# Performance work log

Measured on AMD Instinct MI355X. Metric: run time of the kernel, lower is better.

Reference implementation:

```python
import jax, jax.numpy as jnp
import numpy as np

# ---- SLAYER neuron / simulation params (network.yaml equivalents) ----
THETA = 10.0       # spiking threshold
TAU_SR = 10.0      # synaptic (PSP) alpha-kernel time constant
TAU_REF = 1.0      # refractory alpha-kernel time constant
SCALE_REF = 2.0
TS = 1.0           # simulation step
T_SAMPLE = 350     # number of timesteps

B, NIN, NHID, NOUT = 32, 2312, 512, 10


def _alpha_kernel(tau, mult=1.0, eps=0.01):
    # mirrors slayer._calculateAlphaKernel truncation rule
    ks = []
    for t in np.arange(0.0, T_SAMPLE, TS):
        v = mult * t / tau * np.exp(1.0 - t / tau)
        if abs(v) < eps and t > tau:
            break
        ks.append(v)
    return jnp.asarray(np.asarray(ks, dtype=np.float32))

SRM_KERNEL = _alpha_kernel(TAU_SR)                        # truncated PSP kernel
D_REF = float(np.exp(-TS / TAU_REF))                      # geometric decay of refractory alpha kernel
C_REF = float(-SCALE_REF * THETA * np.e * TS / TAU_REF)   # refKernel[j] = C_REF * j * D_REF**j


def psp(x):
    # causal temporal conv with the SRM alpha kernel, scaled by Ts. x: (B, C, T)
    b, c, t = x.shape
    k = SRM_KERNEL.shape[0]
    out = jax.lax.conv_general_dilated(
        x.reshape(b * c, 1, t), SRM_KERNEL[::-1].reshape(1, 1, k),
        window_strides=(1,), padding=[(k - 1, 0)])
    return (out * TS).reshape(b, c, t)


def spike(u_psp):
    # Sequential thresholding with FULL refractory recurrence: a spike at time s
    # adds refKernel[n-s] = C_REF*(n-s)*D_REF**(n-s) to all future potentials.
    # The alpha kernel is realized EXACTLY by a 2-state linear recurrence (x, y):
    #   x[n] = sum_s spk[s] * d^(n-s),  y[n] = sum_s spk[s] * (n-s) * d^(n-s)
    def step(carry, p_t):
        x, y = carry
        y = D_REF * (y + x)
        u = p_t + C_REF * y           # membrane potential after refractory response
        spk = (u >= THETA).astype(p_t.dtype)
        x = D_REF * x + spk
        return (x, y), spk / TS       # SLAYER emits spikes of magnitude 1/Ts
    b, c, _ = u_psp.shape
    init = (jnp.zeros((b, c), u_psp.dtype), jnp.zeros((b, c), u_psp.dtype))
    _, s = jax.lax.scan(step, init, jnp.moveaxis(u_psp, -1, 0))
    return jnp.moveaxis(s, 0, -1)


def setup_inputs() -> dict:
    key = jax.random.key(0)
    k1, k2, k3 = jax.random.split(key, 3)
    spikeInput = (jax.random.uniform(k1, (B, NIN, T_SAMPLE)) < 0.03).astype(jnp.float32) / TS
    W1 = jax.random.normal(k2, (NHID, NIN), jnp.float32) * 0.05
    W2 = jax.random.normal(k3, (NOUT, NHID), jnp.float32) * 0.5
    return {"spikeInput": spikeInput, "W1": W1, "W2": W2}


def reference(spikeInput, W1, W2):
    # fc (1x1x1 conv == per-timestep matmul) -> psp -> spike, twice
    s1 = spike(psp(jnp.einsum('oi,bit->bot', W1, spikeInput)))
    s2 = spike(psp(jnp.einsum('oi,bit->bot', W2, s1)))
    return s2
```

## Files before the change

kernel.cpp:

```cpp
#include <hip/hip_runtime.h>
#include <hip/hip_bf16.h>
#include <math.h>

#define B_    32
#define NIN_  2312
#define NHID_ 512
#define NOUT_ 10
#define T_    350
#define KLEN  77
#define MW    40
#define NIB   37
#define NTB   6
#define MAXA2 320

__global__ __launch_bounds__(256) void w1t_k(const float* __restrict__ W,
                                             float* __restrict__ WT) {
  __shared__ float tile[32][33];
  int i0 = blockIdx.x * 32, o0 = blockIdx.y * 32;
  int tx = threadIdx.x, tyb = threadIdx.y;
#pragma unroll
  for (int s = 0; s < 4; ++s) {
    int ty = tyb + s * 8;
    int o = o0 + ty, i = i0 + tx;
    if (i < NIN_) tile[ty][tx] = W[(size_t)o * NIN_ + i];
  }
  __syncthreads();
#pragma unroll
  for (int s = 0; s < 4; ++s) {
    int ty = tyb + s * 8;
    int i = i0 + ty, o = o0 + tx;
    if (i < NIN_) WT[(size_t)i * NHID_ + o] = tile[tx][ty];
  }
}

__global__ __launch_bounds__(256) void inmask_k(const float* __restrict__ X,
                                                unsigned long long* __restrict__ msk) {
  __shared__ unsigned evens[64], odds[64];
  int blk = blockIdx.x;
  int iblk = blk % NIB;
  int b = blk / NIB;
  int tid = threadIdx.x;
  int w = tid >> 6, lane = tid & 63;
  int rhalf = lane >> 5;
  int c2 = lane & 31;
  const float* base = X + ((size_t)b * NIN_ + (size_t)iblk * 64) * T_;
  for (int tb = 0; tb < NTB; ++tb) {
    int tbase = tb * 64;
#define PH1_(Q)                                                                \
  {                                                                            \
    int row = 16 * w + 2 * (Q) + rhalf;                                        \
    bool ok = (iblk * 64 + row) < NIN_ && (tbase + 2 * c2) < T_;               \
    const float* rp = base + (size_t)row * T_ + tbase + 2 * c2;                \
    float2 v = ok ? *(const float2*)rp : make_float2(0.f, 0.f);                \
    unsigned long long be = __ballot(v.x != 0.f);                              \
    unsigned long long bo = __ballot(v.y != 0.f);                              \
    if (lane == 0) {                                                           \
      evens[16 * w + 2 * (Q)] = (unsigned)be;                                  \
      odds[16 * w + 2 * (Q)] = (unsigned)bo;                                   \
    }                                                                          \
    if (lane == 1) {                                                           \
      evens[16 * w + 2 * (Q) + 1] = (unsigned)(be >> 32);                      \
      odds[16 * w + 2 * (Q) + 1] = (unsigned)(bo >> 32);                       \
    }                                                                          \
  }
    PH1_(0) PH1_(1) PH1_(2) PH1_(3) PH1_(4) PH1_(5) PH1_(6) PH1_(7)
#undef PH1_
    __syncthreads();
    unsigned ev = evens[lane], od = odds[lane];
    unsigned long long* mrow =
        msk + ((size_t)b * T_ + tbase + w * 16) * MW + iblk;
#define BAL_(P)                                                                \
  {                                                                            \
    unsigned sel = ((P) & 1) ? od : ev;                                        \
    unsigned long long bw_ =                                                   \
        __ballot(((sel >> (w * 8 + ((P) >> 1))) & 1u) != 0u);                  \
    if (lane == (P) && (tbase + w * 16 + (P)) < T_)                            \
      mrow[(size_t)(P) * MW] = bw_;                                            \
  }
    BAL_(0)  BAL_(1)  BAL_(2)  BAL_(3)  BAL_(4)  BAL_(5)  BAL_(6)  BAL_(7)
    BAL_(8)  BAL_(9)  BAL_(10) BAL_(11) BAL_(12) BAL_(13) BAL_(14) BAL_(15)
#undef BAL_
    __syncthreads();
  }
}

__global__ __launch_bounds__(64) void accum1_k(const unsigned long long* __restrict__ msk,
                                               const float* __restrict__ WT,
                                               float* __restrict__ Z1) {
  __shared__ unsigned short list[MAXA2];
  int id = blockIdx.x;
  int bt = id >> 1, oc = id & 1;
  int lane = threadIdx.x;
  unsigned long long wm = (lane < NIB) ? msk[(size_t)bt * MW + lane] : 0ull;
  int pc = __popcll(wm);
  int pre = pc;
#pragma unroll
  for (int d = 1; d < 64; d <<= 1) {
    int o = __shfl_up(pre, d);
    if (lane >= d) pre += o;
  }
  int base = pre - pc;
  int n = __shfl(pre, 63);
  while (wm) {
    int j = __builtin_ctzll(wm);
    if (base < MAXA2) list[base] = (unsigned short)(lane * 64 + j);
    ++base;
    wm &= wm - 1;
  }
  __syncthreads();
  if (n > MAXA2) n = MAXA2;
  const float4* wbase = (const float4*)WT + (size_t)oc * 64 + lane;
  float4 acc = make_float4(0.f, 0.f, 0.f, 0.f);
#pragma unroll 16
  for (int j = 0; j < n; ++j) {
    float4 v = wbase[(size_t)list[j] * (NHID_ / 4)];
    acc.x += v.x;
    acc.y += v.y;
    acc.z += v.z;
    acc.w += v.w;
  }
  ((float4*)(Z1 + (size_t)bt * NHID_))[(size_t)oc * 64 + lane] = acc;
}

__global__ __launch_bounds__(64) void scan1_k(const float* __restrict__ Z1,
                                              unsigned long long* __restrict__ mask) {
  int lane = threadIdx.x;
  int b = blockIdx.x >> 3, g = blockIdx.x & 7;
  int h = g * 64 + lane;
  const double dp   = exp(-0.1);
  const double Ap   = exp(1.0) / 10.0;
  const double D77  = exp(-7.7);
  const float  Dref = (float)exp(-1.0);
  const float  Cref = (float)(-20.0 * exp(1.0));
  double Xc = 0.0, Yc = 0.0, Xd = 0.0, Yd = 0.0;
  float xr = 0.f, yr = 0.f;
  const float* zb = Z1 + (size_t)b * T_ * NHID_ + h;
  unsigned long long* mb = mask + (size_t)b * T_ * 8 + g;
  for (int t0 = 0; t0 < T_; t0 += 16) {
    float z[16], zd[16];
#pragma unroll
    for (int k = 0; k < 16; ++k) {
      int t = t0 + k;
      z[k]  = (t < T_) ? zb[(size_t)t * NHID_] : 0.f;
      zd[k] = (t >= KLEN && t < T_) ? zb[(size_t)(t - KLEN) * NHID_] : 0.f;
    }
#pragma unroll
    for (int k = 0; k < 16; ++k) {
      int t = t0 + k;
      if (t >= T_) break;
      Yc = dp * (Yc + Xc); Xc = dp * Xc + (double)z[k];
      Yd = dp * (Yd + Xd); Xd = dp * Xd + (double)zd[k];
      float p = (float)(Ap * (Yc - D77 * (Yd + 77.0 * Xd)));
      yr = Dref * (yr + xr);
      float u = p + Cref * yr;
      float s = (u >= 10.0f) ? 1.0f : 0.0f;
      xr = Dref * xr + s;
      unsigned long long bw = __ballot(u >= 10.0f);
      if (lane == 0) mb[(size_t)t * 8] = bw;
    }
  }
}

__global__ __launch_bounds__(256) void z2_k(const unsigned long long* __restrict__ mask,
                                            const float* __restrict__ W2,
                                            float* __restrict__ Z2) {
  int wave = blockIdx.x * 4 + (threadIdx.x >> 6);
  int lane = threadIdx.x & 63;
  if (wave >= B_ * T_) return;
  int b = wave / T_, t = wave - b * T_;
  const unsigned long long* m = mask + (size_t)wave * 8;
  if (lane < NOUT_) {
    const float* wr = W2 + (size_t)lane * NHID_;
    float acc = 0.f;
#pragma unroll
    for (int w = 0; w < 8; ++w) {
      unsigned long long mm = m[w];
      while (mm) {
        int j = __builtin_ctzll(mm);
        mm &= mm - 1;
        acc += wr[w * 64 + j];
      }
    }
    Z2[((size_t)b * NOUT_ + lane) * T_ + t] = acc;
  }
}

__global__ __launch_bounds__(64) void scan2_k(const float* __restrict__ Z2,
                                              float* __restrict__ out) {
  int n = blockIdx.x * 64 + threadIdx.x;
  if (n >= B_ * NOUT_) return;
  const double dp   = exp(-0.1);
  const double Ap   = exp(1.0) / 10.0;
  const double D77  = exp(-7.7);
  const float  Dref = (float)exp(-1.0);
  const float  Cref = (float)(-20.0 * exp(1.0));
  double Xc = 0.0, Yc = 0.0, Xd = 0.0, Yd = 0.0;
  float xr = 0.f, yr = 0.f;
  const float* row = Z2 + (size_t)n * T_;
  float* orow = out + (size_t)n * T_;
  for (int t0 = 0; t0 < T_; t0 += 16) {
    float z[16], zd[16];
#pragma unroll
    for (int k = 0; k < 16; ++k) {
      int t = t0 + k;
      z[k]  = (t < T_) ? row[t] : 0.f;
      zd[k] = (t >= KLEN && t < T_) ? row[t - KLEN] : 0.f;
    }
#pragma unroll
    for (int k = 0; k < 16; ++k) {
      int t = t0 + k;
      if (t >= T_) break;
      Yc = dp * (Yc + Xc); Xc = dp * Xc + (double)z[k];
      Yd = dp * (Yd + Xd); Xd = dp * Xd + (double)zd[k];
      float p = (float)(Ap * (Yc - D77 * (Yd + 77.0 * Xd)));
      yr = Dref * (yr + xr);
      float u = p + Cref * yr;
      float s = (u >= 10.0f) ? 1.0f : 0.0f;
      xr = Dref * xr + s;
      orow[t] = s;
    }
  }
}

extern "C" void kernel_launch(void* const* d_in, const int* in_sizes, int n_in,
                              void* d_out, int out_size, void* d_ws, size_t ws_size,
                              hipStream_t stream) {
  const float* X  = (const float*)d_in[0];
  const float* W1 = (const float*)d_in[1];
  const float* W2 = (const float*)d_in[2];
  float* out = (float*)d_out;

  char* ws = (char*)d_ws;
  size_t off = 0;
  float* W1T = (float*)(ws + off);                 off += (size_t)NIN_ * NHID_ * 4;
  unsigned long long* msk = (unsigned long long*)(ws + off); off += (size_t)B_ * T_ * MW * 8;
  float* Z1 = (float*)(ws + off);                  off += (size_t)B_ * T_ * NHID_ * 4;
  unsigned long long* mask = (unsigned long long*)(ws + off); off += (size_t)B_ * T_ * 8 * 8;
  float* Z2 = (float*)(ws + off);                  off += (size_t)B_ * NOUT_ * T_ * 4;
  if (off > ws_size) return;

  w1t_k<<<dim3((NIN_ + 31) / 32, NHID_ / 32), dim3(32, 8), 0, stream>>>(W1, W1T);
  inmask_k<<<B_ * NIB, 256, 0, stream>>>(X, msk);
  accum1_k<<<B_ * T_ * 2, 64, 0, stream>>>(msk, W1T, Z1);
  scan1_k<<<B_ * 8, 64, 0, stream>>>(Z1, mask);
  z2_k<<<(B_ * T_ + 3) / 4, 256, 0, stream>>>(mask, W2, Z2);
  scan2_k<<<(B_ * NOUT_ + 63) / 64, 64, 0, stream>>>(Z2, out);
}
```

Measured before the change: 354.7 us.

## Split PSP convolution from spike scan into time-chunked parallel kernels

```diff
diff --git a/kernel.cpp b/kernel.cpp
--- a/kernel.cpp
+++ b/kernel.cpp
@@ -12,6 +12,8 @@
 #define NIB   37
 #define NTB   6
 #define MAXA2 320
+#define NCH   7
+#define CHL   50
 
 __global__ __launch_bounds__(256) void w1t_k(const float* __restrict__ W,
                                              float* __restrict__ WT) {
@@ -122,37 +124,60 @@
   ((float4*)(Z1 + (size_t)bt * NHID_))[(size_t)oc * 64 + lane] = acc;
 }
 
-__global__ __launch_bounds__(64) void scan1_k(const float* __restrict__ Z1,
-                                              unsigned long long* __restrict__ mask) {
+__global__ __launch_bounds__(64) void psp1_k(const float* __restrict__ Z1,
+                                             float* __restrict__ P1) {
+  int blk = blockIdx.x;
+  int c = blk % NCH;
+  int rem = blk / NCH;
+  int g = rem & 7;
+  int b = rem >> 3;
+  int lane = threadIdx.x;
+  int h = g * 64 + lane;
+  const double dp  = exp(-0.1);
+  const double Ap  = exp(1.0) / 10.0;
+  const double D77 = exp(-7.7);
+  double Xc = 0.0, Yc = 0.0, Xd = 0.0, Yd = 0.0;
+  const float* zb = Z1 + (size_t)b * T_ * NHID_ + h;
+  float* pb = P1 + (size_t)b * T_ * NHID_ + h;
+  int t0 = c * CHL;
+  int s0 = t0 - KLEN; if (s0 < 0) s0 = 0;
+  int tend = t0 + CHL;
+  float zc = zb[(size_t)s0 * NHID_];
+  float zdc = 0.f;
+  for (int t = s0; t < tend; ++t) {
+    int tn = t + 1;
+    float zn  = (tn < tend) ? zb[(size_t)tn * NHID_] : 0.f;
+    float zdn = (tn < tend && tn - KLEN >= s0) ? zb[(size_t)(tn - KLEN) * NHID_] : 0.f;
+    Yc = dp * (Yc + Xc); Xc = dp * Xc + (double)zc;
+    Yd = dp * (Yd + Xd); Xd = dp * Xd + (double)zdc;
+    if (t >= t0) pb[(size_t)t * NHID_] = (float)(Ap * (Yc - D77 * (Yd + 77.0 * Xd)));
+    zc = zn; zdc = zdn;
+  }
+}
+
+__global__ __launch_bounds__(64) void scan1b_k(const float* __restrict__ P1,
+                                               unsigned long long* __restrict__ mask) {
   int lane = threadIdx.x;
   int b = blockIdx.x >> 3, g = blockIdx.x & 7;
   int h = g * 64 + lane;
-  const double dp   = exp(-0.1);
-  const double Ap   = exp(1.0) / 10.0;
-  const double D77  = exp(-7.7);
-  const float  Dref = (float)exp(-1.0);
-  const float  Cref = (float)(-20.0 * exp(1.0));
-  double Xc = 0.0, Yc = 0.0, Xd = 0.0, Yd = 0.0;
+  const float Dref = (float)exp(-1.0);
+  const float Cref = (float)(-20.0 * exp(1.0));
   float xr = 0.f, yr = 0.f;
-  const float* zb = Z1 + (size_t)b * T_ * NHID_ + h;
+  const float* pb = P1 + (size_t)b * T_ * NHID_ + h;
   unsigned long long* mb = mask + (size_t)b * T_ * 8 + g;
   for (int t0 = 0; t0 < T_; t0 += 16) {
-    float z[16], zd[16];
-#pragma unroll
-    for (int k = 0; k < 16; ++k) {
-      int t = t0 + k;
-      z[k]  = (t < T_) ? zb[(size_t)t * NHID_] : 0.f;
-      zd[k] = (t >= KLEN && t < T_) ? zb[(size_t)(t - KLEN) * NHID_] : 0.f;
+    float p[16];
+#pragma unroll
+    for (int k = 0; k < 16; ++k) {
+      int t = t0 + k;
+      p[k] = (t < T_) ? pb[(size_t)t * NHID_] : 0.f;
     }
 #pragma unroll
     for (int k = 0; k < 16; ++k) {
       int t = t0 + k;
       if (t >= T_) break;
-      Yc = dp * (Yc + Xc); Xc = dp * Xc + (double)z[k];
-      Yd = dp * (Yd + Xd); Xd = dp * Xd + (double)zd[k];
-      float p = (float)(Ap * (Yc - D77 * (Yd + 77.0 * Xd)));
       yr = Dref * (yr + xr);
-      float u = p + Cref * yr;
+      float u = p[k] + Cref * yr;
       float s = (u >= 10.0f) ? 1.0f : 0.0f;
       xr = Dref * xr + s;
       unsigned long long bw = __ballot(u >= 10.0f);
@@ -163,7 +188,7 @@
 
 __global__ __launch_bounds__(256) void z2_k(const unsigned long long* __restrict__ mask,
                                             const float* __restrict__ W2,
-                                            float* __restrict__ Z2) {
+                                            float* __restrict__ Z2T) {
   int wave = blockIdx.x * 4 + (threadIdx.x >> 6);
   int lane = threadIdx.x & 63;
   if (wave >= B_ * T_) return;
@@ -181,40 +206,57 @@
         acc += wr[w * 64 + j];
       }
     }
-    Z2[((size_t)b * NOUT_ + lane) * T_ + t] = acc;
-  }
-}
-
-__global__ __launch_bounds__(64) void scan2_k(const float* __restrict__ Z2,
-                                              float* __restrict__ out) {
-  int n = blockIdx.x * 64 + threadIdx.x;
-  if (n >= B_ * NOUT_) return;
-  const double dp   = exp(-0.1);
-  const double Ap   = exp(1.0) / 10.0;
-  const double D77  = exp(-7.7);
-  const float  Dref = (float)exp(-1.0);
-  const float  Cref = (float)(-20.0 * exp(1.0));
+    Z2T[(size_t)t * (B_ * NOUT_) + b * NOUT_ + lane] = acc;
+  }
+}
+
+__global__ __launch_bounds__(320) void psp2_k(const float* __restrict__ Z2T,
+                                              float* __restrict__ P2T) {
+  int n = threadIdx.x;
+  int c = blockIdx.x;
+  const double dp  = exp(-0.1);
+  const double Ap  = exp(1.0) / 10.0;
+  const double D77 = exp(-7.7);
   double Xc = 0.0, Yc = 0.0, Xd = 0.0, Yd = 0.0;
+  const float* zb = Z2T + n;
+  float* pb = P2T + n;
+  int t0 = c * CHL;
+  int s0 = t0 - KLEN; if (s0 < 0) s0 = 0;
+  int tend = t0 + CHL;
+  float zc = zb[(size_t)s0 * (B_ * NOUT_)];
+  float zdc = 0.f;
+  for (int t = s0; t < tend; ++t) {
+    int tn = t + 1;
+    float zn  = (tn < tend) ? zb[(size_t)tn * (B_ * NOUT_)] : 0.f;
+    float zdn = (tn < tend && tn - KLEN >= s0) ? zb[(size_t)(tn - KLEN) * (B_ * NOUT_)] : 0.f;
+    Yc = dp * (Yc + Xc); Xc = dp * Xc + (double)zc;
+    Yd = dp * (Yd + Xd); Xd = dp * Xd + (double)zdc;
+    if (t >= t0) pb[(size_t)t * (B_ * NOUT_)] = (float)(Ap * (Yc - D77 * (Yd + 77.0 * Xd)));
+    zc = zn; zdc = zdn;
+  }
+}
+
+__global__ __launch_bounds__(320) void scan2b_k(const float* __restrict__ P2T,
+                                                float* __restrict__ out) {
+  int n = threadIdx.x;
+  const float Dref = (float)exp(-1.0);
+  const float Cref = (float)(-20.0 * exp(1.0));
   float xr = 0.f, yr = 0.f;
-  const float* row = Z2 + (size_t)n * T_;
+  const float* pb = P2T + n;
   float* orow = out + (size_t)n * T_;
   for (int t0 = 0; t0 < T_; t0 += 16) {
-    float z[16], zd[16];
-#pragma unroll
-    for (int k = 0; k < 16; ++k) {
-      int t = t0 + k;
-      z[k]  = (t < T_) ? row[t] : 0.f;
-      zd[k] = (t >= KLEN && t < T_) ? row[t - KLEN] : 0.f;
+    float p[16];
+#pragma unroll
+    for (int k = 0; k < 16; ++k) {
+      int t = t0 + k;
+      p[k] = (t < T_) ? pb[(size_t)t * (B_ * NOUT_)] : 0.f;
     }
 #pragma unroll
     for (int k = 0; k < 16; ++k) {
       int t = t0 + k;
       if (t >= T_) break;
-      Yc = dp * (Yc + Xc); Xc = dp * Xc + (double)z[k];
-      Yd = dp * (Yd + Xd); Xd = dp * Xd + (double)zd[k];
-      float p = (float)(Ap * (Yc - D77 * (Yd + 77.0 * Xd)));
       yr = Dref * (yr + xr);
-      float u = p + Cref * yr;
+      float u = p[k] + Cref * yr;
       float s = (u >= 10.0f) ? 1.0f : 0.0f;
       xr = Dref * xr + s;
       orow[t] = s;
@@ -235,14 +277,18 @@
   float* W1T = (float*)(ws + off);                 off += (size_t)NIN_ * NHID_ * 4;
   unsigned long long* msk = (unsigned long long*)(ws + off); off += (size_t)B_ * T_ * MW * 8;
   float* Z1 = (float*)(ws + off);                  off += (size_t)B_ * T_ * NHID_ * 4;
+  float* P1 = (float*)(ws + off);                  off += (size_t)B_ * T_ * NHID_ * 4;
   unsigned long long* mask = (unsigned long long*)(ws + off); off += (size_t)B_ * T_ * 8 * 8;
-  float* Z2 = (float*)(ws + off);                  off += (size_t)B_ * NOUT_ * T_ * 4;
+  float* Z2T = (float*)(ws + off);                 off += (size_t)T_ * B_ * NOUT_ * 4;
+  float* P2T = (float*)(ws + off);                 off += (size_t)T_ * B_ * NOUT_ * 4;
   if (off > ws_size) return;
 
   w1t_k<<<dim3((NIN_ + 31) / 32, NHID_ / 32), dim3(32, 8), 0, stream>>>(W1, W1T);
   inmask_k<<<B_ * NIB, 256, 0, stream>>>(X, msk);
   accum1_k<<<B_ * T_ * 2, 64, 0, stream>>>(msk, W1T, Z1);
-  scan1_k<<<B_ * 8, 64, 0, stream>>>(Z1, mask);
-  z2_k<<<(B_ * T_ + 3) / 4, 256, 0, stream>>>(mask, W2, Z2);
-  scan2_k<<<(B_ * NOUT_ + 63) / 64, 64, 0, stream>>>(Z2, out);
-}
+  psp1_k<<<B_ * 8 * NCH, 64, 0, stream>>>(Z1, P1);
+  scan1b_k<<<B_ * 8, 64, 0, stream>>>(P1, mask);
+  z2_k<<<(B_ * T_ + 3) / 4, 256, 0, stream>>>(mask, W2, Z2T);
+  psp2_k<<<NCH, 320, 0, stream>>>(Z2T, P2T);
+  scan2b_k<<<1, 320, 0, stream>>>(P2T, out);
+}
```

Result: slower. 430.9 us (+21.5%).
